# Kernel optimization log

Hardware: AMD Instinct MI355X
Metric: run time of the kernel (lower is better)

## Reference

```python
import jax, jax.numpy as jnp
import numpy as np

TEMPERATURE = 0.07
B, D = 8192, 1024


def setup_inputs() -> dict:
    key = jax.random.key(0)
    k1, k2 = jax.random.split(key)
    audio_embeds = jax.random.normal(k1, (B, D), dtype=jnp.float32)
    text_embeds = jax.random.normal(k2, (B, D), dtype=jnp.float32)
    return {"audio_embeds": audio_embeds, "text_embeds": text_embeds}


def _l2norm(x):
    return x / jnp.linalg.norm(x, axis=-1, keepdims=True)


def reference(audio_embeds, text_embeds):
    # InfoNCE(paired) with leave-one-out negatives + self positive is exactly
    # softmax-CE over the full BxB cosine-similarity matrix with diagonal labels.
    a = _l2norm(audio_embeds)  # [B, D]
    t = _l2norm(text_embeds)   # [B, D]
    sim = jnp.einsum("bd,cd->bc", a, t) / TEMPERATURE  # [B, B]
    # audio->text direction: rows of sim, label = diagonal
    loss_a2t = -jnp.mean(jnp.diagonal(jax.nn.log_softmax(sim, axis=1)))
    # text->audio direction: sim of text queries vs audio keys = sim.T
    loss_t2a = -jnp.mean(jnp.diagonal(jax.nn.log_softmax(sim.T, axis=1)))
    return 0.5 * (loss_a2t + loss_t2a)
```

## Files before the change

### kernel.cpp

```cpp
#include <hip/hip_runtime.h>
#include <stdint.h>

#define D_DIM 1024
#define INV_T 14.2857142857142857f
#define QSCALE 32.0f
#define EPI_SCALE (INV_T / (QSCALE * QSCALE))
#define BK 64
#define NT (D_DIM / BK)

typedef __attribute__((ext_vector_type(4))) float f32x4;

__global__ __launch_bounds__(256) void norm_diag_kernel(
    const float* __restrict__ A, const float* __restrict__ T,
    unsigned int* __restrict__ An, unsigned int* __restrict__ Tn,
    float* __restrict__ diag)
{
  const int row = blockIdx.x;
  const int tid = threadIdx.x;
  const size_t base = (size_t)row * D_DIM;
  const float4 av = ((const float4*)(A + base))[tid];
  const float4 tv = ((const float4*)(T + base))[tid];
  float sa = av.x*av.x + av.y*av.y + av.z*av.z + av.w*av.w;
  float st = tv.x*tv.x + tv.y*tv.y + tv.z*tv.z + tv.w*tv.w;
  float sd = av.x*tv.x + av.y*tv.y + av.z*tv.z + av.w*tv.w;
  #pragma unroll
  for (int m = 1; m < 64; m <<= 1) {
    sa += __shfl_xor(sa, m, 64);
    st += __shfl_xor(st, m, 64);
    sd += __shfl_xor(sd, m, 64);
  }
  __shared__ float red[3][4];
  const int wid = tid >> 6;
  if ((tid & 63) == 0) { red[0][wid] = sa; red[1][wid] = st; red[2][wid] = sd; }
  __syncthreads();
  sa = red[0][0] + red[0][1] + red[0][2] + red[0][3];
  st = red[1][0] + red[1][1] + red[1][2] + red[1][3];
  sd = red[2][0] + red[2][1] + red[2][2] + red[2][3];
  const float ra = rsqrtf(sa), rt = rsqrtf(st);
  if (tid == 0) diag[row] = sd * ra * rt * INV_T;
  const float qa = ra * QSCALE, qt = rt * QSCALE;
  unsigned int ao = __builtin_amdgcn_cvt_pk_fp8_f32(av.x*qa, av.y*qa, 0, 0);
  ao = __builtin_amdgcn_cvt_pk_fp8_f32(av.z*qa, av.w*qa, ao, 1);
  unsigned int to = __builtin_amdgcn_cvt_pk_fp8_f32(tv.x*qt, tv.y*qt, 0, 0);
  to = __builtin_amdgcn_cvt_pk_fp8_f32(tv.z*qt, tv.w*qt, to, 1);
  An[row * 256 + tid] = ao;
  Tn[row * 256 + tid] = to;
}

__device__ __forceinline__ void gload_lds16(const void* g, void* l) {
  __builtin_amdgcn_global_load_lds(
      (const __attribute__((address_space(1))) unsigned int*)g,
      (__attribute__((address_space(3))) unsigned int*)l, 16, 0, 0);
}

#define SBAR asm volatile("s_barrier" ::: "memory")

#define STAGE2(T) do {                                                          \
    const unsigned char* _a = aP + (size_t)(T) * BK;                            \
    const unsigned char* _b = bP + (size_t)(T) * BK;                            \
    const int _bb = ((T) & 1) * 16384;                                          \
    _Pragma("unroll")                                                           \
    for (int _i = 0; _i < 2; ++_i) {                                            \
      const int _ci = _i*256 + tid;                                             \
      const int _r = _ci >> 2, _c = _ci & 3;                                    \
      const size_t _go = (size_t)_r * D_DIM + ((_c ^ ((_r >> 1) & 3)) << 4);    \
      gload_lds16(_a + _go, &lds[_bb + _ci*16]);                                \
      gload_lds16(_b + _go, &lds[_bb + 8192 + _ci*16]);                         \
    }                                                                           \
  } while (0)

__global__ __launch_bounds__(256, 4) void gemm_lse_kernel(
    const unsigned char* __restrict__ An, const unsigned char* __restrict__ Tn,
    float* __restrict__ Srow, float* __restrict__ Scol, int nbc)
{
  __shared__ unsigned char lds[32768];

  const int nwg = gridDim.x;
  const int bid = blockIdx.x;
  const int cpx = nwg >> 3;
  const int swz = (bid & 7) * cpx + (bid >> 3);
  const int brow = swz / nbc;
  const int bcol = swz - brow * nbc;

  const int tid  = threadIdx.x;
  const int lane = tid & 63;
  const int wid  = tid >> 6;
  const int wr   = wid >> 1, wc = wid & 1;
  const int lcol = lane & 15, lrow = lane >> 4;

  const unsigned char* aP = An + (size_t)brow * 128 * D_DIM;
  const unsigned char* bP = Tn + (size_t)bcol * 128 * D_DIM;

  f32x4 acc[4][4] = {};

  STAGE2(0);
  STAGE2(1);
  asm volatile("s_waitcnt vmcnt(4)" ::: "memory");
  SBAR;

  for (int t = 0; t < NT; ++t) {
    const int bb = (t & 1) * 16384;
    #pragma unroll
    for (int kk = 0; kk < 2; ++kk) {
      long af[4], bfr[4];
      #pragma unroll
      for (int m = 0; m < 4; ++m) {
        const int row = wr*64 + m*16 + lcol;
        const int s = (kk*4 + lrow) ^ (row & 6);
        af[m] = *(const long*)&lds[bb + row*64 + s*8];
      }
      #pragma unroll
      for (int n = 0; n < 4; ++n) {
        const int row = wc*64 + n*16 + lcol;
        const int s = (kk*4 + lrow) ^ (row & 6);
        bfr[n] = *(const long*)&lds[bb + 8192 + row*64 + s*8];
      }
      #pragma unroll
      for (int m = 0; m < 4; ++m)
        #pragma unroll
        for (int n = 0; n < 4; ++n)
          acc[m][n] = __builtin_amdgcn_mfma_f32_16x16x32_fp8_fp8(af[m], bfr[n], acc[m][n], 0, 0, 0);
    }
    SBAR;
    if (t + 2 < NT) {
      STAGE2(t + 2);
      asm volatile("s_waitcnt vmcnt(4)" ::: "memory");
    } else {
      asm volatile("s_waitcnt vmcnt(0)" ::: "memory");
    }
    SBAR;
  }

  float rowsum[4][4];
  float colsum[4];
  #pragma unroll
  for (int m = 0; m < 4; ++m)
    #pragma unroll
    for (int r = 0; r < 4; ++r) rowsum[m][r] = 0.f;
  #pragma unroll
  for (int n = 0; n < 4; ++n) {
    float cs = 0.f;
    #pragma unroll
    for (int m = 0; m < 4; ++m)
      #pragma unroll
      for (int r = 0; r < 4; ++r) {
        const float e = __expf(acc[m][n][r] * EPI_SCALE);
        rowsum[m][r] += e;
        cs += e;
      }
    colsum[n] = cs;
  }
  #pragma unroll
  for (int m = 0; m < 4; ++m)
    #pragma unroll
    for (int r = 0; r < 4; ++r) {
      float v = rowsum[m][r];
      v += __shfl_xor(v, 1, 64);
      v += __shfl_xor(v, 2, 64);
      v += __shfl_xor(v, 4, 64);
      v += __shfl_xor(v, 8, 64);
      if (lcol == 0)
        atomicAdd(&Srow[brow*128 + wr*64 + m*16 + lrow*4 + r], v);
    }
  #pragma unroll
  for (int n = 0; n < 4; ++n) {
    float v = colsum[n];
    v += __shfl_xor(v, 16, 64);
    v += __shfl_xor(v, 32, 64);
    if (lane < 16)
      atomicAdd(&Scol[bcol*128 + wc*64 + n*16 + lcol], v);
  }
}

__global__ __launch_bounds__(256) void loss_kernel(
    const float* __restrict__ Srow, const float* __restrict__ Scol,
    const float* __restrict__ diag, float* __restrict__ out, int B)
{
  float s = 0.f;
  for (int i = threadIdx.x; i < B; i += 256)
    s += 0.5f * (__logf(Srow[i]) + __logf(Scol[i])) - diag[i];
  #pragma unroll
  for (int m = 1; m < 64; m <<= 1) s += __shfl_xor(s, m, 64);
  __shared__ float red[4];
  if ((threadIdx.x & 63) == 0) red[threadIdx.x >> 6] = s;
  __syncthreads();
  if (threadIdx.x == 0) out[0] = (red[0] + red[1] + red[2] + red[3]) / (float)B;
}

extern "C" void kernel_launch(void* const* d_in, const int* in_sizes, int n_in,
                              void* d_out, int out_size, void* d_ws, size_t ws_size,
                              hipStream_t stream) {
  const float* A = (const float*)d_in[0];
  const float* T = (const float*)d_in[1];
  const int B = in_sizes[0] / D_DIM;
  const int nbc = B / 128;

  char* ws = (char*)d_ws;
  unsigned char* An = (unsigned char*)ws;
  unsigned char* Tn = An + (size_t)B * D_DIM;
  float* Srow = (float*)(ws + (size_t)2 * B * D_DIM);
  float* Scol = Srow + B;
  float* diag = Scol + B;

  hipMemsetAsync(Srow, 0, (size_t)2 * B * sizeof(float), stream);
  norm_diag_kernel<<<B, 256, 0, stream>>>(A, T, (unsigned int*)An, (unsigned int*)Tn, diag);
  gemm_lse_kernel<<<nbc * nbc, 256, 0, stream>>>(An, Tn, Srow, Scol, nbc);
  loss_kernel<<<1, 256, 0, stream>>>(Srow, Scol, diag, (float*)d_out, B);
}
```

Baseline: 169.7 us.

## Switch GEMM to 16x16x128 scaled FP8 MFMA with 128-wide K stages

Replaces the 16x16x32 FP8 MFMA with the gfx950 scaled 16x16x128 f8f6f4 MFMA using unit scales. K stages widen from 64 to 128 bytes, so LDS doubles to 64KB, the XOR swizzle is rewritten for 8 chunks, and the loop is fully unrolled over 8 stages. Occupancy drops from 4 to 2 workgroups per CU. It also raises wave priority around the MFMA block. The intent is fewer MFMA issues and fewer barriers per K, at the cost of occupancy and more register pressure.

```diff
diff --git a/kernel.cpp b/kernel.cpp
--- a/kernel.cpp
+++ b/kernel.cpp
@@ -5,10 +5,11 @@
 #define INV_T 14.2857142857142857f
 #define QSCALE 32.0f
 #define EPI_SCALE (INV_T / (QSCALE * QSCALE))
-#define BK 64
-#define NT (D_DIM / BK)
+#define NP 8
 
 typedef __attribute__((ext_vector_type(4))) float f32x4;
+typedef __attribute__((ext_vector_type(4))) int i32x4;
+typedef __attribute__((ext_vector_type(8))) int i32x8;
 
 __global__ __launch_bounds__(256) void norm_diag_kernel(
     const float* __restrict__ A, const float* __restrict__ T,
@@ -55,25 +56,25 @@
 
 #define SBAR asm volatile("s_barrier" ::: "memory")
 
-#define STAGE2(T) do {                                                          \
-    const unsigned char* _a = aP + (size_t)(T) * BK;                            \
-    const unsigned char* _b = bP + (size_t)(T) * BK;                            \
-    const int _bb = ((T) & 1) * 16384;                                          \
+#define STAGE_PAIR(S, BP) do {                                                  \
+    const unsigned char* _a = aP + (size_t)(S) * 128;                           \
+    const unsigned char* _b = bP + (size_t)(S) * 128;                           \
+    const int _bb = (BP) * 32768;                                               \
     _Pragma("unroll")                                                           \
-    for (int _i = 0; _i < 2; ++_i) {                                            \
+    for (int _i = 0; _i < 4; ++_i) {                                            \
       const int _ci = _i*256 + tid;                                             \
-      const int _r = _ci >> 2, _c = _ci & 3;                                    \
-      const size_t _go = (size_t)_r * D_DIM + ((_c ^ ((_r >> 1) & 3)) << 4);    \
+      const int _r = _ci >> 3, _c = _ci & 7;                                    \
+      const size_t _go = (size_t)_r * D_DIM + ((_c ^ (_r & 7)) << 4);           \
       gload_lds16(_a + _go, &lds[_bb + _ci*16]);                                \
-      gload_lds16(_b + _go, &lds[_bb + 8192 + _ci*16]);                         \
+      gload_lds16(_b + _go, &lds[_bb + 16384 + _ci*16]);                        \
     }                                                                           \
   } while (0)
 
-__global__ __launch_bounds__(256, 4) void gemm_lse_kernel(
+__global__ __launch_bounds__(256, 2) void gemm_lse_kernel(
     const unsigned char* __restrict__ An, const unsigned char* __restrict__ Tn,
     float* __restrict__ Srow, float* __restrict__ Scol, int nbc)
 {
-  __shared__ unsigned char lds[32768];
+  __shared__ unsigned char lds[65536];
 
   const int nwg = gridDim.x;
   const int bid = blockIdx.x;
@@ -93,38 +94,49 @@
 
   f32x4 acc[4][4] = {};
 
-  STAGE2(0);
-  STAGE2(1);
-  asm volatile("s_waitcnt vmcnt(4)" ::: "memory");
+  STAGE_PAIR(0, 0);
+  STAGE_PAIR(1, 1);
+  asm volatile("s_waitcnt vmcnt(8)" ::: "memory");
   SBAR;
 
-  for (int t = 0; t < NT; ++t) {
-    const int bb = (t & 1) * 16384;
-    #pragma unroll
-    for (int kk = 0; kk < 2; ++kk) {
-      long af[4], bfr[4];
+  #pragma unroll
+  for (int s = 0; s < NP; ++s) {
+    const int bb = (s & 1) * 32768;
+    i32x8 af[4], bf[4];
+    #pragma unroll
+    for (int m = 0; m < 4; ++m) {
+      const int row = wr*64 + m*16 + lcol;
+      const int c0 = lrow ^ (row & 7);
+      const int c1 = (4 + lrow) ^ (row & 7);
+      const i32x4 lo = *(const i32x4*)&lds[bb + row*128 + c0*16];
+      const i32x4 hi = *(const i32x4*)&lds[bb + row*128 + c1*16];
+      af[m][0]=lo[0]; af[m][1]=lo[1]; af[m][2]=lo[2]; af[m][3]=lo[3];
+      af[m][4]=hi[0]; af[m][5]=hi[1]; af[m][6]=hi[2]; af[m][7]=hi[3];
+    }
+    #pragma unroll
+    for (int n = 0; n < 4; ++n) {
+      const int row = wc*64 + n*16 + lcol;
+      const int c0 = lrow ^ (row & 7);
+      const int c1 = (4 + lrow) ^ (row & 7);
+      const i32x4 lo = *(const i32x4*)&lds[bb + 16384 + row*128 + c0*16];
+      const i32x4 hi = *(const i32x4*)&lds[bb + 16384 + row*128 + c1*16];
+      bf[n][0]=lo[0]; bf[n][1]=lo[1]; bf[n][2]=lo[2]; bf[n][3]=lo[3];
+      bf[n][4]=hi[0]; bf[n][5]=hi[1]; bf[n][6]=hi[2]; bf[n][7]=hi[3];
+    }
+    __builtin_amdgcn_s_setprio(1);
+    #pragma unroll
+    for (int m = 0; m < 4; ++m)
       #pragma unroll
-      for (int m = 0; m < 4; ++m) {
-        const int row = wr*64 + m*16 + lcol;
-        const int s = (kk*4 + lrow) ^ (row & 6);
-        af[m] = *(const long*)&lds[bb + row*64 + s*8];
-      }
-      #pragma unroll
-      for (int n = 0; n < 4; ++n) {
-        const int row = wc*64 + n*16 + lcol;
-        const int s = (kk*4 + lrow) ^ (row & 6);
-        bfr[n] = *(const long*)&lds[bb + 8192 + row*64 + s*8];
-      }
-      #pragma unroll
-      for (int m = 0; m < 4; ++m)
-        #pragma unroll
-        for (int n = 0; n < 4; ++n)
-          acc[m][n] = __builtin_amdgcn_mfma_f32_16x16x32_fp8_fp8(af[m], bfr[n], acc[m][n], 0, 0, 0);
-    }
+      for (int n = 0; n < 4; ++n)
+        acc[m][n] = __builtin_amdgcn_mfma_scale_f32_16x16x128_f8f6f4(
+            af[m], bf[n], acc[m][n], 0, 0,
+            0, 0x7F7F7F7F, 0, 0x7F7F7F7F);
+    __builtin_amdgcn_s_setprio(0);
+    asm volatile("s_waitcnt lgkmcnt(0)" ::: "memory");
     SBAR;
-    if (t + 2 < NT) {
-      STAGE2(t + 2);
-      asm volatile("s_waitcnt vmcnt(4)" ::: "memory");
+    if (s + 2 < NP) {
+      STAGE_PAIR(s + 2, s & 1);
+      asm volatile("s_waitcnt vmcnt(8)" ::: "memory");
     } else {
       asm volatile("s_waitcnt vmcnt(0)" ::: "memory");
     }
```

Measured after the change: 513.4 us. 3.03x slower.
